# Optimization experiments

Measured on AMD Instinct MI355X. Metric: run time of the kernel, lower is better.

## Reference

```python
import jax, jax.numpy as jnp
import numpy as np

HIST_SIZE = 200
DIM = 64
HIDDEN = 32
NEG_INF = -2.0**32 + 1.0  # matches tf padding constant


def setup_inputs() -> dict:
    key = jax.random.key(0)
    k1, k2, k3, k4, k5 = jax.random.split(key, 5)
    B = 4096
    cand = jax.random.normal(k1, (B, DIM), dtype=jnp.float32)
    hist = jax.random.normal(k2, (B, HIST_SIZE, DIM), dtype=jnp.float32)
    hisLens = jax.random.randint(k3, (B,), 0, HIST_SIZE, dtype=jnp.int32)
    # Glorot-normal-ish params
    attW1 = jax.random.normal(k4, (4 * DIM, HIDDEN), dtype=jnp.float32) * (2.0 / (4 * DIM + HIDDEN)) ** 0.5
    attB1 = jnp.zeros((HIDDEN,), dtype=jnp.float32)
    attW2 = jax.random.normal(k5, (HIDDEN, 1), dtype=jnp.float32) * (2.0 / (HIDDEN + 1)) ** 0.5
    attB2 = jnp.zeros((1,), dtype=jnp.float32)
    return {"candidate_embedding": cand, "hist_embeddings": hist, "hisLens": hisLens,
            "attW1": attW1, "attB1": attB1, "attW2": attW2, "attB2": attB2}


def reference(candidate_embedding, hist_embeddings, hisLens, attW1, attB1, attW2, attB2):
    # candidate: [B, d] -> broadcast over hist steps [B, S, d]
    cand = candidate_embedding[:, None, :]
    # per-step feature concat: [cand, hist, cand*hist, cand-hist] -> [B, S, 4d]
    z3 = jnp.concatenate([
        jnp.broadcast_to(cand, hist_embeddings.shape),
        hist_embeddings,
        cand * hist_embeddings,
        cand - hist_embeddings,
    ], axis=-1)
    # tiny 2-layer MLP scorer -> [B, S]
    h = jax.nn.relu(jnp.einsum('bsf,fh->bsh', z3, attW1) + attB1)
    scores = (jnp.einsum('bsh,ho->bso', h, attW2) + attB2)[..., 0]
    # sequence mask then scale (same order as original), softmax over hist dim
    mask = jnp.arange(HIST_SIZE)[None, :] < hisLens[:, None]
    scores = jnp.where(mask, scores, NEG_INF) / (DIM ** 0.5)
    w = jax.nn.softmax(scores, axis=-1)  # [B, S]
    # weighted sum of history embeddings -> [B, d]
    return jnp.einsum('bs,bsd->bd', w, hist_embeddings)
```

## Files before the change

### kernel.cpp

```cpp
#include <hip/hip_runtime.h>
#include <math.h>

#define HS    200
#define DIMV  64
#define HID   32
#define NTH   512

typedef __attribute__((ext_vector_type(8))) short short8;
typedef __attribute__((ext_vector_type(4))) float f32x4;
typedef __bf16 bf2_t __attribute__((ext_vector_type(2)));
typedef float  f2_t  __attribute__((ext_vector_type(2)));

__device__ __forceinline__ unsigned cvt2(float x, float y) {
    f2_t f = {x, y};
    bf2_t bv = __builtin_convertvector(f, bf2_t);
    union { bf2_t b; unsigned u; } un;
    un.b = bv;
    return un.u;
}
__device__ __forceinline__ float bf16f(short x) {
    return __uint_as_float(((unsigned)(unsigned short)x) << 16);
}

template<int CTRL>
__device__ __forceinline__ float dpp_add(float x) {
    int y = __builtin_amdgcn_update_dpp(0, __float_as_int(x), CTRL, 0xF, 0xF, true);
    return x + __int_as_float(y);
}
template<int CTRL>
__device__ __forceinline__ float dpp_max(float x) {
    int y = __builtin_amdgcn_update_dpp(0, __float_as_int(x), CTRL, 0xF, 0xF, true);
    return fmaxf(x, __int_as_float(y));
}
#define ROR1  0x121
#define ROR2  0x122
#define ROR4  0x124
#define ROR8  0x128
#define QXOR1 0xB1
#define QXOR2 0x4E
#define HMIRR 0x141
__device__ __forceinline__ float swz_xor16(float x) {
    return __int_as_float(__builtin_amdgcn_ds_swizzle(__float_as_int(x), 0x401F));
}


__global__ __launch_bounds__(NTH, 8) void din_attn_kernel(
    const float* __restrict__ cand,
    const float* __restrict__ hist,
    const int*   __restrict__ lens,
    const float* __restrict__ W1,
    const float* __restrict__ B1,
    const float* __restrict__ W2,
    const float* __restrict__ B2,
    float* __restrict__ out)
{
    __shared__ __align__(16) unsigned short s_h[208 * 64];
    __shared__ __align__(16) unsigned char  s_u[4096];
    __shared__ float s_sc[208];
    __shared__ float s_c[HID];
    __shared__ float s_w2[HID];

    unsigned short* s_Mt   = (unsigned short*)s_u;
    float*          s_part = (float*)s_u;

    const int b   = blockIdx.x;
    const int tid = threadIdx.x;
    const int lane = tid & 63, wid = tid >> 6;
    const float* cb = cand + (size_t)b * DIMV;

    const int len  = lens[b];
    const int nrow = (len == 0) ? HS : len;
    const int npairs = nrow * 8;

    const float4* hp = (const float4*)(hist + (size_t)b * (HS * DIMV));
    float4 va[4], vb[4];
    #pragma unroll
    for (int j = 0; j < 4; ++j) {
        int pi = tid + j * NTH;
        if (pi < npairs) {
            va[j] = hp[2 * pi];
            vb[j] = hp[2 * pi + 1];
        }
    }

    if (tid < 256) {
        const int h = tid & 31, fg = tid >> 5;
        float4 cA = *(const float4*)(cb + fg * 8);
        float4 cB = *(const float4*)(cb + fg * 8 + 4);
        float cf[8] = {cA.x, cA.y, cA.z, cA.w, cB.x, cB.y, cB.z, cB.w};
        float m[8];
        #pragma unroll
        for (int ff = 0; ff < 8; ++ff) {
            int f = fg * 8 + ff;
            m[ff] = W1[(DIMV + f) * HID + h]
                  - W1[(3 * DIMV + f) * HID + h]
                  + cf[ff] * W1[(2 * DIMV + f) * HID + h];
        }
        uint4 mw = make_uint4(cvt2(m[0], m[1]), cvt2(m[2], m[3]),
                              cvt2(m[4], m[5]), cvt2(m[6], m[7]));
        int pg = fg ^ (h & 7);
        *(uint4*)&s_Mt[h * 64 + pg * 8] = mw;
        if (tid < HID) s_w2[tid] = W2[tid];
    } else {
        const int t2 = tid - 256;
        const int h = t2 >> 3, fg = t2 & 7;
        float p = 0.f;
        #pragma unroll
        for (int ff = 0; ff < 8; ++ff) {
            int f = fg * 8 + ff;
            p += cb[f] * (W1[f * HID + h] + W1[(3 * DIMV + f) * HID + h]);
        }
        p = dpp_add<QXOR1>(p);
        p = dpp_add<QXOR2>(p);
        p = dpp_add<HMIRR>(p);
        if ((tid & 7) == 0) s_c[h] = p + B1[h];
    }

    #pragma unroll
    for (int j = 0; j < 4; ++j) {
        int pi = tid + j * NTH;
        if (pi < npairs) {
            int r = pi >> 3, g = pi & 7;
            int pg = g ^ (r & 7);
            uint4 w = make_uint4(cvt2(va[j].x, va[j].y), cvt2(va[j].z, va[j].w),
                                 cvt2(vb[j].x, vb[j].y), cvt2(vb[j].z, vb[j].w));
            *(uint4*)&s_h[r * 64 + pg * 8] = w;
        }
    }
    __syncthreads();

    {
        const int nt = (len + 15) >> 4;
        const int lc = lane & 15, lg = lane >> 4;
        const float c0  = s_c[lc],  c1  = s_c[16 + lc];
        const float w20 = s_w2[lc], w21 = s_w2[16 + lc];

        short8 b00 = *(const short8*)&s_Mt[lc * 64        + ((lg)     ^ (lc & 7)) * 8];
        short8 b01 = *(const short8*)&s_Mt[lc * 64        + ((4 + lg) ^ (lc & 7)) * 8];
        short8 b10 = *(const short8*)&s_Mt[(16 + lc) * 64 + ((lg)     ^ (lc & 7)) * 8];
        short8 b11 = *(const short8*)&s_Mt[(16 + lc) * 64 + ((4 + lg) ^ (lc & 7)) * 8];

        for (int rt = wid; rt < nt; rt += 8) {
            int s = rt * 16 + lc;
            s = (s < len) ? s : (len - 1);
            short8 a0 = *(const short8*)&s_h[s * 64 + ((lg)     ^ (s & 7)) * 8];
            short8 a1 = *(const short8*)&s_h[s * 64 + ((4 + lg) ^ (s & 7)) * 8];
            f32x4 acc0 = {c0, c0, c0, c0};
            acc0 = __builtin_amdgcn_mfma_f32_16x16x32_bf16(a0, b00, acc0, 0, 0, 0);
            acc0 = __builtin_amdgcn_mfma_f32_16x16x32_bf16(a1, b01, acc0, 0, 0, 0);
            f32x4 acc1 = {c1, c1, c1, c1};
            acc1 = __builtin_amdgcn_mfma_f32_16x16x32_bf16(a0, b10, acc1, 0, 0, 0);
            acc1 = __builtin_amdgcn_mfma_f32_16x16x32_bf16(a1, b11, acc1, 0, 0, 0);
            float p[4];
            #pragma unroll
            for (int r = 0; r < 4; ++r)
                p[r] = fmaxf(acc0[r], 0.f) * w20 + fmaxf(acc1[r], 0.f) * w21;
            #pragma unroll
            for (int r = 0; r < 4; ++r) {
                p[r] = dpp_add<ROR1>(p[r]);
                p[r] = dpp_add<ROR2>(p[r]);
                p[r] = dpp_add<ROR4>(p[r]);
                p[r] = dpp_add<ROR8>(p[r]);
            }
            if (lc == 0) {
                int rbase = rt * 16 + lg * 4;
                #pragma unroll
                for (int r = 0; r < 4; ++r) s_sc[rbase + r] = p[r];
            }
        }
    }
    __syncthreads();

    if (wid == 0) {
        float xs[4];
        #pragma unroll
        for (int j = 0; j < 4; ++j) {
            int s = j * 64 + lane;
            if (len == 0) xs[j] = (s < HS) ? 0.f : -INFINITY;
            else          xs[j] = (s < len) ? s_sc[s] * 0.125f : -INFINITY;
        }
        float mx = fmaxf(fmaxf(xs[0], xs[1]), fmaxf(xs[2], xs[3]));
        mx = dpp_max<ROR1>(mx); mx = dpp_max<ROR2>(mx);
        mx = dpp_max<ROR4>(mx); mx = dpp_max<ROR8>(mx);
        mx = fmaxf(mx, swz_xor16(mx));
        mx = fmaxf(mx, __shfl_xor(mx, 32));
        float e[4];
        float sm = 0.f;
        #pragma unroll
        for (int j = 0; j < 4; ++j) { e[j] = __expf(xs[j] - mx); sm += e[j]; }
        sm = dpp_add<ROR1>(sm); sm = dpp_add<ROR2>(sm);
        sm = dpp_add<ROR4>(sm); sm = dpp_add<ROR8>(sm);
        sm += swz_xor16(sm);
        sm += __shfl_xor(sm, 32);
        const float inv = 1.0f / sm;
        #pragma unroll
        for (int j = 0; j < 4; ++j) {
            int s = j * 64 + lane;
            if (s < HS) s_sc[s] = e[j] * inv;
        }
    }
    __syncthreads();

    {
        const int nrb = (nrow + 7) >> 3;
        float a3[8] = {0.f, 0.f, 0.f, 0.f, 0.f, 0.f, 0.f, 0.f};
        for (int rb = wid; rb < nrb; rb += 8) {
            int s = rb * 8 + (lane >> 3);
            float wgt = (s < nrow) ? s_sc[s] : 0.f;
            s = (s < nrow) ? s : (nrow - 1);
            int g = lane & 7;
            short8 hv = *(const short8*)&s_h[s * 64 + (g ^ (s & 7)) * 8];
            #pragma unroll
            for (int j = 0; j < 8; ++j) a3[j] = fmaf(wgt, bf16f(hv[j]), a3[j]);
        }
        #pragma unroll
        for (int j = 0; j < 8; ++j) {
            float x = dpp_add<ROR8>(a3[j]);
            x += swz_xor16(x);
            x += __shfl_xor(x, 32);
            a3[j] = x;
        }
        if (lane < 8) {
            float* dst = &s_part[wid * 64 + lane * 8];
            *(float4*)dst       = make_float4(a3[0], a3[1], a3[2], a3[3]);
            *(float4*)(dst + 4) = make_float4(a3[4], a3[5], a3[6], a3[7]);
        }
    }
    __syncthreads();
    if (tid < DIMV) {
        float res = 0.f;
        #pragma unroll
        for (int k = 0; k < 8; ++k) res += s_part[k * 64 + tid];
        out[(size_t)b * DIMV + tid] = res;
    }
}

extern "C" void kernel_launch(void* const* d_in, const int* in_sizes, int n_in,
                              void* d_out, int out_size, void* d_ws, size_t ws_size,
                              hipStream_t stream) {
    const float* cand = (const float*)d_in[0];
    const float* hist = (const float*)d_in[1];
    const int*   lens = (const int*)d_in[2];
    const float* W1   = (const float*)d_in[3];
    const float* B1   = (const float*)d_in[4];
    const float* W2   = (const float*)d_in[5];
    const float* B2   = (const float*)d_in[6];
    float* out = (float*)d_out;

    const int B = in_sizes[0] / DIMV;
    din_attn_kernel<<<B, NTH, 0, stream>>>(cand, hist, lens, W1, B1, W2, B2, out);
}
```

Before: 39.23 us.

## Process four batch rows per block with prefetch of next row's history

Each block now loops over four batch elements (strided by grid size) and issues global loads for the next element's history into registers while computing scores for the current one. The per-block W1 weight combinations are hoisted into registers once and reused, and the M/c matrices are double-buffered in LDS. This aims to hide global load latency and amortize setup, at the cost of fewer blocks (B/4), higher register pressure, and occupancy bound lowered to 4. It assumes B is divisible by 4.

```diff
diff --git a/kernel.cpp b/kernel.cpp
--- a/kernel.cpp
+++ b/kernel.cpp
@@ -5,6 +5,7 @@
 #define DIMV  64
 #define HID   32
 #define NTH   512
+#define NB    4
 
 typedef __attribute__((ext_vector_type(8))) short short8;
 typedef __attribute__((ext_vector_type(4))) float f32x4;
@@ -44,7 +45,7 @@
 }
 
 
-__global__ __launch_bounds__(NTH, 8) void din_attn_kernel(
+__global__ __launch_bounds__(NTH, 4) void din_attn_kernel(
     const float* __restrict__ cand,
     const float* __restrict__ hist,
     const int*   __restrict__ lens,
@@ -55,183 +56,223 @@
     float* __restrict__ out)
 {
     __shared__ __align__(16) unsigned short s_h[208 * 64];
-    __shared__ __align__(16) unsigned char  s_u[4096];
+    __shared__ __align__(16) unsigned short s_Mt[2][HID * 64];
     __shared__ float s_sc[208];
-    __shared__ float s_c[HID];
+    __shared__ float s_c[2][HID];
     __shared__ float s_w2[HID];
-
-    unsigned short* s_Mt   = (unsigned short*)s_u;
-    float*          s_part = (float*)s_u;
-
-    const int b   = blockIdx.x;
-    const int tid = threadIdx.x;
+    __shared__ __align__(16) float s_part[8 * DIMV];
+
+    const int tid  = threadIdx.x;
     const int lane = tid & 63, wid = tid >> 6;
-    const float* cb = cand + (size_t)b * DIMV;
-
-    const int len  = lens[b];
-    const int nrow = (len == 0) ? HS : len;
-    const int npairs = nrow * 8;
-
-    const float4* hp = (const float4*)(hist + (size_t)b * (HS * DIMV));
-    float4 va[4], vb[4];
-    #pragma unroll
-    for (int j = 0; j < 4; ++j) {
-        int pi = tid + j * NTH;
-        if (pi < npairs) {
-            va[j] = hp[2 * pi];
-            vb[j] = hp[2 * pi + 1];
-        }
-    }
-
+    const int GRID = gridDim.x;
+
+    const int h_m = tid & 31, fg_m = tid >> 5;
+    const int t2  = tid - 256;
+    const int h_c = t2 >> 3, fg_c = t2 & 7;
+    float wbd[8], wcc[8];
+    float wad[8];
+    float b1h = 0.f;
     if (tid < 256) {
-        const int h = tid & 31, fg = tid >> 5;
-        float4 cA = *(const float4*)(cb + fg * 8);
-        float4 cB = *(const float4*)(cb + fg * 8 + 4);
-        float cf[8] = {cA.x, cA.y, cA.z, cA.w, cB.x, cB.y, cB.z, cB.w};
-        float m[8];
         #pragma unroll
         for (int ff = 0; ff < 8; ++ff) {
-            int f = fg * 8 + ff;
-            m[ff] = W1[(DIMV + f) * HID + h]
-                  - W1[(3 * DIMV + f) * HID + h]
-                  + cf[ff] * W1[(2 * DIMV + f) * HID + h];
-        }
-        uint4 mw = make_uint4(cvt2(m[0], m[1]), cvt2(m[2], m[3]),
-                              cvt2(m[4], m[5]), cvt2(m[6], m[7]));
-        int pg = fg ^ (h & 7);
-        *(uint4*)&s_Mt[h * 64 + pg * 8] = mw;
+            int f = fg_m * 8 + ff;
+            wbd[ff] = W1[(DIMV + f) * HID + h_m] - W1[(3 * DIMV + f) * HID + h_m];
+            wcc[ff] = W1[(2 * DIMV + f) * HID + h_m];
+        }
         if (tid < HID) s_w2[tid] = W2[tid];
     } else {
-        const int t2 = tid - 256;
-        const int h = t2 >> 3, fg = t2 & 7;
-        float p = 0.f;
         #pragma unroll
         for (int ff = 0; ff < 8; ++ff) {
-            int f = fg * 8 + ff;
-            p += cb[f] * (W1[f * HID + h] + W1[(3 * DIMV + f) * HID + h]);
-        }
-        p = dpp_add<QXOR1>(p);
-        p = dpp_add<QXOR2>(p);
-        p = dpp_add<HMIRR>(p);
-        if ((tid & 7) == 0) s_c[h] = p + B1[h];
+            int f = fg_c * 8 + ff;
+            wad[ff] = W1[f * HID + h_c] + W1[(3 * DIMV + f) * HID + h_c];
+        }
+        b1h = B1[h_c];
     }
 
+    int lenk[NB];
     #pragma unroll
-    for (int j = 0; j < 4; ++j) {
-        int pi = tid + j * NTH;
-        if (pi < npairs) {
-            int r = pi >> 3, g = pi & 7;
-            int pg = g ^ (r & 7);
-            uint4 w = make_uint4(cvt2(va[j].x, va[j].y), cvt2(va[j].z, va[j].w),
-                                 cvt2(vb[j].x, vb[j].y), cvt2(vb[j].z, vb[j].w));
-            *(uint4*)&s_h[r * 64 + pg * 8] = w;
-        }
+    for (int k = 0; k < NB; ++k) lenk[k] = lens[blockIdx.x + k * GRID];
+
+    float4 va[4], vb[4];
+
+    auto issueLoads = [&](int b, int npairs) {
+        const float4* hp = (const float4*)(hist + (size_t)b * (HS * DIMV));
+        #pragma unroll
+        for (int j = 0; j < 4; ++j) {
+            int pi = tid + j * NTH;
+            if (pi < npairs) { va[j] = hp[2 * pi]; vb[j] = hp[2 * pi + 1]; }
+        }
+    };
+    auto writeLDS = [&](int npairs) {
+        #pragma unroll
+        for (int j = 0; j < 4; ++j) {
+            int pi = tid + j * NTH;
+            if (pi < npairs) {
+                int r = pi >> 3, g = pi & 7;
+                int pg = g ^ (r & 7);
+                uint4 w = make_uint4(cvt2(va[j].x, va[j].y), cvt2(va[j].z, va[j].w),
+                                     cvt2(vb[j].x, vb[j].y), cvt2(vb[j].z, vb[j].w));
+                *(uint4*)&s_h[r * 64 + pg * 8] = w;
+            }
+        }
+    };
+    auto phaseA = [&](int b, int bi) {
+        const float* cbk = cand + (size_t)b * DIMV;
+        if (tid < 256) {
+            float4 cA = *(const float4*)(cbk + fg_m * 8);
+            float4 cB = *(const float4*)(cbk + fg_m * 8 + 4);
+            float cf[8] = {cA.x, cA.y, cA.z, cA.w, cB.x, cB.y, cB.z, cB.w};
+            float m[8];
+            #pragma unroll
+            for (int ff = 0; ff < 8; ++ff) m[ff] = fmaf(cf[ff], wcc[ff], wbd[ff]);
+            uint4 mw = make_uint4(cvt2(m[0], m[1]), cvt2(m[2], m[3]),
+                                  cvt2(m[4], m[5]), cvt2(m[6], m[7]));
+            int pg = fg_m ^ (h_m & 7);
+            *(uint4*)&s_Mt[bi][h_m * 64 + pg * 8] = mw;
+        } else {
+            float4 cA = *(const float4*)(cbk + fg_c * 8);
+            float4 cB = *(const float4*)(cbk + fg_c * 8 + 4);
+            float cf[8] = {cA.x, cA.y, cA.z, cA.w, cB.x, cB.y, cB.z, cB.w};
+            float p = 0.f;
+            #pragma unroll
+            for (int ff = 0; ff < 8; ++ff) p = fmaf(cf[ff], wad[ff], p);
+            p = dpp_add<QXOR1>(p);
+            p = dpp_add<QXOR2>(p);
+            p = dpp_add<HMIRR>(p);
+            if ((t2 & 7) == 0) s_c[bi][h_c] = p + b1h;
+        }
+    };
+
+    {
+        int len0  = lenk[0];
+        int nrow0 = (len0 == 0) ? HS : len0;
+        issueLoads(blockIdx.x, nrow0 * 8);
+        phaseA(blockIdx.x, 0);
+        writeLDS(nrow0 * 8);
     }
     __syncthreads();
 
-    {
-        const int nt = (len + 15) >> 4;
-        const int lc = lane & 15, lg = lane >> 4;
-        const float c0  = s_c[lc],  c1  = s_c[16 + lc];
-        const float w20 = s_w2[lc], w21 = s_w2[16 + lc];
-
-        short8 b00 = *(const short8*)&s_Mt[lc * 64        + ((lg)     ^ (lc & 7)) * 8];
-        short8 b01 = *(const short8*)&s_Mt[lc * 64        + ((4 + lg) ^ (lc & 7)) * 8];
-        short8 b10 = *(const short8*)&s_Mt[(16 + lc) * 64 + ((lg)     ^ (lc & 7)) * 8];
-        short8 b11 = *(const short8*)&s_Mt[(16 + lc) * 64 + ((4 + lg) ^ (lc & 7)) * 8];
-
-        for (int rt = wid; rt < nt; rt += 8) {
-            int s = rt * 16 + lc;
-            s = (s < len) ? s : (len - 1);
-            short8 a0 = *(const short8*)&s_h[s * 64 + ((lg)     ^ (s & 7)) * 8];
-            short8 a1 = *(const short8*)&s_h[s * 64 + ((4 + lg) ^ (s & 7)) * 8];
-            f32x4 acc0 = {c0, c0, c0, c0};
-            acc0 = __builtin_amdgcn_mfma_f32_16x16x32_bf16(a0, b00, acc0, 0, 0, 0);
-            acc0 = __builtin_amdgcn_mfma_f32_16x16x32_bf16(a1, b01, acc0, 0, 0, 0);
-            f32x4 acc1 = {c1, c1, c1, c1};
-            acc1 = __builtin_amdgcn_mfma_f32_16x16x32_bf16(a0, b10, acc1, 0, 0, 0);
-            acc1 = __builtin_amdgcn_mfma_f32_16x16x32_bf16(a1, b11, acc1, 0, 0, 0);
-            float p[4];
-            #pragma unroll
-            for (int r = 0; r < 4; ++r)
-                p[r] = fmaxf(acc0[r], 0.f) * w20 + fmaxf(acc1[r], 0.f) * w21;
-            #pragma unroll
-            for (int r = 0; r < 4; ++r) {
-                p[r] = dpp_add<ROR1>(p[r]);
-                p[r] = dpp_add<ROR2>(p[r]);
-                p[r] = dpp_add<ROR4>(p[r]);
-                p[r] = dpp_add<ROR8>(p[r]);
-            }
-            if (lc == 0) {
-                int rbase = rt * 16 + lg * 4;
+    #pragma unroll
+    for (int k = 0; k < NB; ++k) {
+        const int b    = blockIdx.x + k * GRID;
+        const int len  = lenk[k];
+        const int nrow = (len == 0) ? HS : len;
+        const int kn   = k + 1;
+        int nrown = 0;
+        if (kn < NB) {
+            int lenn = lenk[kn];
+            nrown = (lenn == 0) ? HS : lenn;
+            issueLoads(blockIdx.x + kn * GRID, nrown * 8);
+        }
+
+        {
+            const int nt = (len + 15) >> 4;
+            const int lc = lane & 15, lg = lane >> 4;
+            const float c0  = s_c[k & 1][lc],  c1  = s_c[k & 1][16 + lc];
+            const float w20 = s_w2[lc],        w21 = s_w2[16 + lc];
+            const unsigned short* mt = s_Mt[k & 1];
+            short8 b00 = *(const short8*)&mt[lc * 64        + ((lg)     ^ (lc & 7)) * 8];
+            short8 b01 = *(const short8*)&mt[lc * 64        + ((4 + lg) ^ (lc & 7)) * 8];
+            short8 b10 = *(const short8*)&mt[(16 + lc) * 64 + ((lg)     ^ (lc & 7)) * 8];
+            short8 b11 = *(const short8*)&mt[(16 + lc) * 64 + ((4 + lg) ^ (lc & 7)) * 8];
+
+            for (int rt = wid; rt < nt; rt += 8) {
+                int s = rt * 16 + lc;
+                s = (s < len) ? s : (len - 1);
+                short8 a0 = *(const short8*)&s_h[s * 64 + ((lg)     ^ (s & 7)) * 8];
+                short8 a1 = *(const short8*)&s_h[s * 64 + ((4 + lg) ^ (s & 7)) * 8];
+                f32x4 acc0 = {c0, c0, c0, c0};
+                acc0 = __builtin_amdgcn_mfma_f32_16x16x32_bf16(a0, b00, acc0, 0, 0, 0);
+                acc0 = __builtin_amdgcn_mfma_f32_16x16x32_bf16(a1, b01, acc0, 0, 0, 0);
+                f32x4 acc1 = {c1, c1, c1, c1};
+                acc1 = __builtin_amdgcn_mfma_f32_16x16x32_bf16(a0, b10, acc1, 0, 0, 0);
+                acc1 = __builtin_amdgcn_mfma_f32_16x16x32_bf16(a1, b11, acc1, 0, 0, 0);
+                float p[4];
                 #pragma unroll
-                for (int r = 0; r < 4; ++r) s_sc[rbase + r] = p[r];
-            }
-        }
-    }
-    __syncthreads();
-
-    if (wid == 0) {
-        float xs[4];
-        #pragma unroll
-        for (int j = 0; j < 4; ++j) {
-            int s = j * 64 + lane;
-            if (len == 0) xs[j] = (s < HS) ? 0.f : -INFINITY;
-            else          xs[j] = (s < len) ? s_sc[s] * 0.125f : -INFINITY;
-        }
-        float mx = fmaxf(fmaxf(xs[0], xs[1]), fmaxf(xs[2], xs[3]));
-        mx = dpp_max<ROR1>(mx); mx = dpp_max<ROR2>(mx);
-        mx = dpp_max<ROR4>(mx); mx = dpp_max<ROR8>(mx);
-        mx = fmaxf(mx, swz_xor16(mx));
-        mx = fmaxf(mx, __shfl_xor(mx, 32));
-        float e[4];
-        float sm = 0.f;
-        #pragma unroll
-        for (int j = 0; j < 4; ++j) { e[j] = __expf(xs[j] - mx); sm += e[j]; }
-        sm = dpp_add<ROR1>(sm); sm = dpp_add<ROR2>(sm);
-        sm = dpp_add<ROR4>(sm); sm = dpp_add<ROR8>(sm);
-        sm += swz_xor16(sm);
-        sm += __shfl_xor(sm, 32);
-        const float inv = 1.0f / sm;
-        #pragma unroll
-        for (int j = 0; j < 4; ++j) {
-            int s = j * 64 + lane;
-            if (s < HS) s_sc[s] = e[j] * inv;
-        }
-    }
-    __syncthreads();
-
-    {
-        const int nrb = (nrow + 7) >> 3;
-        float a3[8] = {0.f, 0.f, 0.f, 0.f, 0.f, 0.f, 0.f, 0.f};
-        for (int rb = wid; rb < nrb; rb += 8) {
-            int s = rb * 8 + (lane >> 3);
-            float wgt = (s < nrow) ? s_sc[s] : 0.f;
-            s = (s < nrow) ? s : (nrow - 1);
-            int g = lane & 7;
-            short8 hv = *(const short8*)&s_h[s * 64 + (g ^ (s & 7)) * 8];
-            #pragma unroll
-            for (int j = 0; j < 8; ++j) a3[j] = fmaf(wgt, bf16f(hv[j]), a3[j]);
-        }
-        #pragma unroll
-        for (int j = 0; j < 8; ++j) {
-            float x = dpp_add<ROR8>(a3[j]);
-            x += swz_xor16(x);
-            x += __shfl_xor(x, 32);
-            a3[j] = x;
-        }
-        if (lane < 8) {
-            float* dst = &s_part[wid * 64 + lane * 8];
-            *(float4*)dst       = make_float4(a3[0], a3[1], a3[2], a3[3]);
-            *(float4*)(dst + 4) = make_float4(a3[4], a3[5], a3[6], a3[7]);
-        }
-    }
-    __syncthreads();
-    if (tid < DIMV) {
-        float res = 0.f;
-        #pragma unroll
-        for (int k = 0; k < 8; ++k) res += s_part[k * 64 + tid];
-        out[(size_t)b * DIMV + tid] = res;
+                for (int r = 0; r < 4; ++r)
+                    p[r] = fmaxf(acc0[r], 0.f) * w20 + fmaxf(acc1[r], 0.f) * w21;
+                #pragma unroll
+                for (int r = 0; r < 4; ++r) {
+                    p[r] = dpp_add<ROR1>(p[r]);
+                    p[r] = dpp_add<ROR2>(p[r]);
+                    p[r] = dpp_add<ROR4>(p[r]);
+                    p[r] = dpp_add<ROR8>(p[r]);
+                }
+                if (lc == 0) {
+                    int rbase = rt * 16 + lg * 4;
+                    #pragma unroll
+                    for (int r = 0; r < 4; ++r) s_sc[rbase + r] = p[r];
+                }
+            }
+        }
+        if (kn < NB) phaseA(blockIdx.x + kn * GRID, kn & 1);
+        __syncthreads();
+
+        if (wid == 0) {
+            float xs[4];
+            #pragma unroll
+            for (int j = 0; j < 4; ++j) {
+                int s = j * 64 + lane;
+                if (len == 0) xs[j] = (s < HS) ? 0.f : -INFINITY;
+                else          xs[j] = (s < len) ? s_sc[s] * 0.125f : -INFINITY;
+            }
+            float mx = fmaxf(fmaxf(xs[0], xs[1]), fmaxf(xs[2], xs[3]));
+            mx = dpp_max<ROR1>(mx); mx = dpp_max<ROR2>(mx);
+            mx = dpp_max<ROR4>(mx); mx = dpp_max<ROR8>(mx);
+            mx = fmaxf(mx, swz_xor16(mx));
+            mx = fmaxf(mx, __shfl_xor(mx, 32));
+            float e[4];
+            float sm = 0.f;
+            #pragma unroll
+            for (int j = 0; j < 4; ++j) { e[j] = __expf(xs[j] - mx); sm += e[j]; }
+            sm = dpp_add<ROR1>(sm); sm = dpp_add<ROR2>(sm);
+            sm = dpp_add<ROR4>(sm); sm = dpp_add<ROR8>(sm);
+            sm += swz_xor16(sm);
+            sm += __shfl_xor(sm, 32);
+            const float inv = 1.0f / sm;
+            #pragma unroll
+            for (int j = 0; j < 4; ++j) {
+                int s = j * 64 + lane;
+                if (s < HS) s_sc[s] = e[j] * inv;
+            }
+        }
+        __syncthreads();
+
+        {
+            const int nrb = (nrow + 7) >> 3;
+            float a3[8] = {0.f, 0.f, 0.f, 0.f, 0.f, 0.f, 0.f, 0.f};
+            for (int rb = wid; rb < nrb; rb += 8) {
+                int s = rb * 8 + (lane >> 3);
+                float wgt = (s < nrow) ? s_sc[s] : 0.f;
+                s = (s < nrow) ? s : (nrow - 1);
+                int g = lane & 7;
+                short8 hv = *(const short8*)&s_h[s * 64 + (g ^ (s & 7)) * 8];
+                #pragma unroll
+                for (int j = 0; j < 8; ++j) a3[j] = fmaf(wgt, bf16f(hv[j]), a3[j]);
+            }
+            #pragma unroll
+            for (int j = 0; j < 8; ++j) {
+                float x = dpp_add<ROR8>(a3[j]);
+                x += swz_xor16(x);
+                x += __shfl_xor(x, 32);
+                a3[j] = x;
+            }
+            if (lane < 8) {
+                float* dst = &s_part[wid * 64 + lane * 8];
+                *(float4*)dst       = make_float4(a3[0], a3[1], a3[2], a3[3]);
+                *(float4*)(dst + 4) = make_float4(a3[4], a3[5], a3[6], a3[7]);
+            }
+        }
+        __syncthreads();
+
+        if (kn < NB) writeLDS(nrown * 8);
+        if (tid < DIMV) {
+            float res = 0.f;
+            #pragma unroll
+            for (int q = 0; q < 8; ++q) res += s_part[q * 64 + tid];
+            out[(size_t)b * DIMV + tid] = res;
+        }
+        __syncthreads();
     }
 }
 
@@ -248,5 +289,6 @@
     float* out = (float*)d_out;
 
     const int B = in_sizes[0] / DIMV;
-    din_attn_kernel<<<B, NTH, 0, stream>>>(cand, hist, lens, W1, B1, W2, B2, out);
-}
+    const int GRID = B / NB;
+    din_attn_kernel<<<GRID, NTH, 0, stream>>>(cand, hist, lens, W1, B1, W2, B2, out);
+}
```

After: 42.58 us. +8.6%, slower.
